# Kernel optimization log

Measured on AMD Instinct MI355X. Metric: run time of the kernel, lower is better.

## Reference

```python
import jax, jax.numpy as jnp
import numpy as np

B, T, E, V, L, BLK = 2, 2048, 1024, 32000, 12, 2048


def setup_inputs() -> dict:
    key = jax.random.key(0)
    ks = jax.random.split(key, 10)
    std = 0.005  # FHE-friendly tiny init, matches nn.init.normal_(std=0.005)
    init = lambda k, shape: jax.random.normal(k, shape, jnp.float32) * std
    return {
        "idx": jax.random.randint(ks[0], (B, T), 0, V, dtype=jnp.int32),
        "wte": init(ks[1], (V, E)),
        "wpe": init(ks[2], (BLK, E)),
        "ln1_w": jnp.ones((L, E), jnp.float32),   # FHELayerNorm weights init to ones
        "Wq": init(ks[3], (L, E, E)),
        "Wk": init(ks[4], (L, E, E)),
        "Wv": init(ks[5], (L, E, E)),
        "Wo": init(ks[6], (L, E, E)),
        "ln2_w": jnp.ones((L, E), jnp.float32),
        "fc1": init(ks[7], (L, 2 * E, E)),
        "fc2": init(ks[8], (L, E, 2 * E)),
        "lnf_w": jnp.ones((E,), jnp.float32),
        "lm_head": init(ks[9], (V, E)),
    }


def reference(idx, wte, wpe, ln1_w, Wq, Wk, Wv, Wo, ln2_w, fc1, fc2, lnf_w, lm_head):
    t = idx.shape[1]
    # embeddings, each scaled by 0.01
    x = wte[idx] * 0.01 + (wpe[:t] * 0.01)[None, :, :]  # [B,T,E]

    n_layer = ln1_w.shape[0]
    # inter-block rescale: 0.1 after every block except the last
    scales = jnp.where(jnp.arange(n_layer) < n_layer - 1, 0.1, 1.0).astype(x.dtype)

    def block(x, p):
        ln1, wq, wk, wv, wo, ln2, f1, f2, s = p
        # FHELayerNorm: pure scaling
        h = x * ln1 * 0.1
        # attention (single head over full E, softmax-free quadratic weights)
        q = jnp.einsum('bte,fe->btf', h, wq) * 0.01
        k = jnp.einsum('bte,fe->btf', h, wk) * 0.01
        v = jnp.einsum('bte,fe->btf', h, wv) * 0.1
        a = jnp.einsum('btf,bsf->bts', q, k) * 0.01      # [B,T,T]
        a = a * a * 0.1 + a * 0.1                         # pointwise quadratic
        ao = jnp.einsum('bts,bsf->btf', a, v) * 0.01
        attn_out = jnp.einsum('btf,ef->bte', ao, wo) * 0.1
        x = (x * 0.5 + attn_out * 0.5) * 0.1
        # MLP with polynomial activation
        h2 = x * ln2 * 0.1
        m = jnp.einsum('bte,fe->btf', h2, f1) * 0.05      # [B,T,2E]
        m = m * m * 0.1 + m * 0.1
        m = jnp.einsum('btf,ef->bte', m, f2) * 0.05
        x = (x * 0.5 + m * 0.5) * 0.1
        return x * s, None

    x, _ = jax.lax.scan(block, x, (ln1_w, Wq, Wk, Wv, Wo, ln2_w, fc1, fc2, scales))
    x = x * lnf_w * 0.1  # final FHELayerNorm
    logits = jnp.einsum('bte,ve->btv', x, lm_head) * 0.5
    return logits
```

## Files before the change

### kernel.cpp

```cpp
#include <hip/hip_runtime.h>
#include <hip/hip_fp8.h>
#include <stdint.h>
#include <math.h>

typedef unsigned short u16;
typedef __attribute__((ext_vector_type(8))) short bf16x8;
typedef __attribute__((ext_vector_type(4))) float f32x4;
typedef __attribute__((ext_vector_type(2))) long long llx2;

typedef __attribute__((address_space(1))) const uint32_t gas_u32;
typedef __attribute__((address_space(3))) uint32_t las_u32;

__device__ __forceinline__ u16 f2b(float f) {
  union { float f; uint32_t u; } v; v.f = f;
  uint32_t r = v.u + 0x7FFFu + ((v.u >> 16) & 1u);
  return (u16)(r >> 16);
}
__device__ __forceinline__ float b2f(u16 b) {
  union { uint32_t u; float f; } v; v.u = ((uint32_t)b) << 16; return v.f;
}
__device__ __forceinline__ uint8_t f8(float x) {
  __hip_fp8_e4m3 t(x);
  return (uint8_t)t.__x;
}
__device__ __forceinline__ int ipos(int k) {
  return (k & ~63) | (k & 7) | ((k & 32) >> 2) | ((k & 24) << 1);
}

__device__ __forceinline__ void gl_lds16(const void* g, void* l) {
  __builtin_amdgcn_global_load_lds((gas_u32*)g, (las_u32*)l, 16, 0, 0);
}
__device__ __forceinline__ void barrier_raw() {
  asm volatile("" ::: "memory");
  __builtin_amdgcn_s_barrier();
  asm volatile("" ::: "memory");
}

#define MM(A_, B_, C_)  __builtin_amdgcn_mfma_f32_16x16x32_bf16(A_, B_, C_, 0, 0, 0)
#define MM8(A_, B_, C_) __builtin_amdgcn_mfma_f32_16x16x32_fp8_fp8(A_, B_, C_, 0, 0, 0)

struct GP {
  const u16* A; long long asb;
  const u16* B[3]; long long bsb;
  u16* O[3]; long long osb;
  int M, N, K, lda, ldb, ldo;
  float alpha[3];
  int epi[3];
  int nsel, msel;
  float* fout; int ldf;
};

template <int MI>
__device__ __forceinline__ void epi_store(const GP& p, u16* __restrict__ Op, float alpha, int epi,
                                          int rbase0, int colb, const f32x4 (&acc)[MI][4], int l4, int l15) {
#pragma unroll
  for (int mi = 0; mi < MI; ++mi) {
    const int rbase = rbase0 + mi * 16 + l4 * 4;
#pragma unroll
    for (int ni = 0; ni < 4; ++ni) {
      const int col = colb + ni * 16 + l15;
      f32x4 v = acc[mi][ni];
#pragma unroll
      for (int r = 0; r < 4; ++r)
        Op[(size_t)(rbase + r) * p.ldo + col] = f2b(v[r] * alpha);
    }
  }
}

__device__ __forceinline__ void xcd_swz(int nwg, int orig, int gx, int& bx, int& by) {
  const int xcd = orig & 7, rem = orig >> 3;
  const int qq = nwg >> 3, rr = nwg & 7;
  const int wg = (xcd < rr ? xcd * (qq + 1) : rr * (qq + 1) + (xcd - rr) * qq) + rem;
  bx = wg % gx; by = wg / gx;
}

#define RD_A(off) do { \
  a0 = *(const bf16x8*)(Abase + (off));        a1 = *(const bf16x8*)(Abase + (off) + 1024); \
  a2 = *(const bf16x8*)(Abase + (off) + 2048); a3 = *(const bf16x8*)(Abase + (off) + 3072); \
} while (0)
#define RD_B(off) do { \
  b0 = *(const bf16x8*)(Bbase + (off));        b1 = *(const bf16x8*)(Bbase + (off) + 1024); \
  b2 = *(const bf16x8*)(Bbase + (off) + 2048); b3 = *(const bf16x8*)(Bbase + (off) + 3072); \
} while (0)
#define MF16(R) do { \
  acc[R+0][0]=MM(a0,b0,acc[R+0][0]); acc[R+0][1]=MM(a0,b1,acc[R+0][1]); acc[R+0][2]=MM(a0,b2,acc[R+0][2]); acc[R+0][3]=MM(a0,b3,acc[R+0][3]); \
  acc[R+1][0]=MM(a1,b0,acc[R+1][0]); acc[R+1][1]=MM(a1,b1,acc[R+1][1]); acc[R+1][2]=MM(a1,b2,acc[R+1][2]); acc[R+1][3]=MM(a1,b3,acc[R+1][3]); \
  acc[R+2][0]=MM(a2,b0,acc[R+2][0]); acc[R+2][1]=MM(a2,b1,acc[R+2][1]); acc[R+2][2]=MM(a2,b2,acc[R+2][2]); acc[R+2][3]=MM(a2,b3,acc[R+2][3]); \
  acc[R+3][0]=MM(a3,b0,acc[R+3][0]); acc[R+3][1]=MM(a3,b1,acc[R+3][1]); acc[R+3][2]=MM(a3,b2,acc[R+3][2]); acc[R+3][3]=MM(a3,b3,acc[R+3][3]); \
} while (0)

#define PHASE_MID() do { \
  asm volatile("s_waitcnt lgkmcnt(0)" ::: "memory"); \
  __builtin_amdgcn_sched_barrier(0); \
  __builtin_amdgcn_s_setprio(1); \
} while (0)
#define PHASE_END() do { \
  __builtin_amdgcn_s_setprio(0); \
  __builtin_amdgcn_sched_barrier(0); \
  barrier_raw(); \
} while (0)

#define SSA(q, kh, t) do { \
  gl_lds16(gA0 + (size_t)(t) * 64 + (kh) * 32, lAw + (q) * 32768 + (kh) * 8192); \
  gl_lds16(gA1 + (size_t)(t) * 64 + (kh) * 32, lAw + (q) * 32768 + (kh) * 8192 + 4096); \
} while (0)
#define SSB(q, kh, t) do { \
  gl_lds16(gB0 + (size_t)(t) * 64 + (kh) * 32, lBw + (q) * 32768 + (kh) * 8192); \
  gl_lds16(gB1 + (size_t)(t) * 64 + (kh) * 32, lBw + (q) * 32768 + (kh) * 8192 + 4096); \
} while (0)

__global__ __launch_bounds__(256, 2) void gemmS_k(GP p) {
  extern __shared__ __attribute__((aligned(16))) char lds[];
  const int z = blockIdx.z;
  int bx, by;
  xcd_swz(gridDim.x * gridDim.y, blockIdx.y * gridDim.x + blockIdx.x, gridDim.x, bx, by);
  const int m0 = bx * 128, n0 = by * 128;
  const u16* __restrict__ Ap = p.A + (size_t)z * p.asb;
  const u16* __restrict__ Bp = p.B[0] + (size_t)z * p.bsb;

  const int tid = threadIdx.x, wid = tid >> 6, lane = tid & 63;
  const int wm = wid >> 1, wn = wid & 1;
  const int l15 = lane & 15, l4 = lane >> 4;
  const int cswz16 = (l4 ^ ((l15 >> 1) & 3)) * 16;

  const f32x4 vzero = {0.f, 0.f, 0.f, 0.f};
  f32x4 acc[4][4];
#pragma unroll
  for (int i = 0; i < 4; ++i)
#pragma unroll
    for (int j = 0; j < 4; ++j) acc[i][j] = vzero;

  const int sr = lane >> 2;
  const int cg8 = ((lane & 3) ^ ((lane >> 3) & 3)) * 8;
  const u16* gA0 = Ap + (size_t)(m0 + wid * 16 + sr) * p.lda + cg8;
  const u16* gA1 = gA0 + (size_t)64 * p.lda;
  const u16* gB0 = Bp + (size_t)(n0 + wid * 16 + sr) * p.ldb + cg8;
  const u16* gB1 = gB0 + (size_t)64 * p.ldb;
  char* lAw = lds + wid * 1024;
  char* lBw = lds + 16384 + wid * 1024;

  const int nt = p.K >> 6;

  SSA(0, 0, 0); SSB(0, 0, 0); SSA(0, 1, 0); SSB(0, 1, 0);
  SSA(1, 0, 1); SSB(1, 0, 1);
  asm volatile("s_waitcnt vmcnt(4)" ::: "memory");
  barrier_raw();

  bf16x8 a0, a1, a2, a3, b0, b1, b2, b3;
  for (int t = 0; t < nt; ++t) {
    const int q = t & 1;
    const char* Abase = lds + q * 32768 + (wm * 64 + l15) * 64 + cswz16;
    const char* Bbase = lds + q * 32768 + 16384 + (wn * 64 + l15) * 64 + cswz16;
    RD_A(0); RD_B(0);
    if (t + 1 < nt) { SSA(q ^ 1, 1, t + 1); SSB(q ^ 1, 1, t + 1); }
    PHASE_MID(); MF16(0); PHASE_END();
    RD_A(8192); RD_B(8192);
    if (t + 2 < nt) { SSA(q, 0, t + 2); SSB(q, 0, t + 2); }
    PHASE_MID(); MF16(0);
    __builtin_amdgcn_s_setprio(0);
    __builtin_amdgcn_sched_barrier(0);
    if (t + 2 < nt) asm volatile("s_waitcnt vmcnt(4)" ::: "memory");
    else            asm volatile("s_waitcnt vmcnt(0)" ::: "memory");
    barrier_raw();
  }

  u16* Op = p.O[0] + (size_t)z * p.osb;
  epi_store<4>(p, Op, p.alpha[0], p.epi[0], m0 + wm * 64, n0 + wn * 64, acc, l4, l15);
}

struct GP8 {
  const uint8_t* A; long long asb;
  const uint8_t* B[3]; long long bsb;
  uint8_t* O[3]; long long osb;
  int K, lda, ldb, ldo;
  float m1[3], m2[3];
  int epi[3];
  int nsel, msel, nfirst;
  float qc;
  float* xres; const float* lnw; float rscale; float oscale;
  uint8_t* h8out;
  float* fout; int ldf;
};

#define S8A(q, kh, t) do { \
  gl_lds16(gA0 + (size_t)(t) * 128 + (kh) * 64, lAw + (q) * 32768 + (kh) * 8192); \
  gl_lds16(gA1 + (size_t)(t) * 128 + (kh) * 64, lAw + (q) * 32768 + (kh) * 8192 + 4096); \
} while (0)
#define S8B(q, kh, t) do { \
  gl_lds16(gB0 + (size_t)(t) * 128 + (kh) * 64, lBw + (q) * 32768 + (kh) * 8192); \
  gl_lds16(gB1 + (size_t)(t) * 128 + (kh) * 64, lBw + (q) * 32768 + (kh) * 8192 + 4096); \
} while (0)

#define MF8() do { \
  acc[0][0]=MM8(a0[0],b0[0],acc[0][0]); acc[0][0]=MM8(a0[1],b0[1],acc[0][0]); \
  acc[0][1]=MM8(a0[0],b1[0],acc[0][1]); acc[0][1]=MM8(a0[1],b1[1],acc[0][1]); \
  acc[0][2]=MM8(a0[0],b2[0],acc[0][2]); acc[0][2]=MM8(a0[1],b2[1],acc[0][2]); \
  acc[0][3]=MM8(a0[0],b3[0],acc[0][3]); acc[0][3]=MM8(a0[1],b3[1],acc[0][3]); \
  acc[1][0]=MM8(a1[0],b0[0],acc[1][0]); acc[1][0]=MM8(a1[1],b0[1],acc[1][0]); \
  acc[1][1]=MM8(a1[0],b1[0],acc[1][1]); acc[1][1]=MM8(a1[1],b1[1],acc[1][1]); \
  acc[1][2]=MM8(a1[0],b2[0],acc[1][2]); acc[1][2]=MM8(a1[1],b2[1],acc[1][2]); \
  acc[1][3]=MM8(a1[0],b3[0],acc[1][3]); acc[1][3]=MM8(a1[1],b3[1],acc[1][3]); \
  acc[2][0]=MM8(a2[0],b0[0],acc[2][0]); acc[2][0]=MM8(a2[1],b0[1],acc[2][0]); \
  acc[2][1]=MM8(a2[0],b1[0],acc[2][1]); acc[2][1]=MM8(a2[1],b1[1],acc[2][1]); \
  acc[2][2]=MM8(a2[0],b2[0],acc[2][2]); acc[2][2]=MM8(a2[1],b2[1],acc[2][2]); \
  acc[2][3]=MM8(a2[0],b3[0],acc[2][3]); acc[2][3]=MM8(a2[1],b3[1],acc[2][3]); \
  acc[3][0]=MM8(a3[0],b0[0],acc[3][0]); acc[3][0]=MM8(a3[1],b0[1],acc[3][0]); \
  acc[3][1]=MM8(a3[0],b1[0],acc[3][1]); acc[3][1]=MM8(a3[1],b1[1],acc[3][1]); \
  acc[3][2]=MM8(a3[0],b2[0],acc[3][2]); acc[3][2]=MM8(a3[1],b2[1],acc[3][2]); \
  acc[3][3]=MM8(a3[0],b3[0],acc[3][3]); acc[3][3]=MM8(a3[1],b3[1],acc[3][3]); \
} while (0)

__global__ __launch_bounds__(256, 2) void gemm8_k(GP8 p) {
  extern __shared__ __attribute__((aligned(16))) char lds[];
  const int z = blockIdx.z;
  int bx, by;
  xcd_swz(gridDim.x * gridDim.y, blockIdx.y * gridDim.x + blockIdx.x, gridDim.x, bx, by);
  const int m0 = p.nfirst ? by * 128 : bx * 128;
  const int n0 = p.nfirst ? bx * 128 : by * 128;
  const int zi = p.nsel ? (n0 >> 10) : 0;
  const int nB = p.nsel ? (n0 & 1023) : n0;
  const uint8_t* __restrict__ Ap = p.A + (size_t)z * p.asb;
  const uint8_t* __restrict__ Bp = p.B[zi] + (size_t)(p.msel ? (m0 >> 11) : z) * p.bsb;

  const int tid = threadIdx.x, wid = tid >> 6, lane = tid & 63;
  const int wm = wid >> 1, wn = wid & 1;
  const int l15 = lane & 15, l4 = lane >> 4;
  const int cswz16 = (l4 ^ ((l15 >> 1) & 3)) * 16;

  const f32x4 vzero = {0.f, 0.f, 0.f, 0.f};
  f32x4 acc[4][4];
#pragma unroll
  for (int i = 0; i < 4; ++i)
#pragma unroll
    for (int j = 0; j < 4; ++j) acc[i][j] = vzero;

  const int sr = lane >> 2;
  const int cgB = ((lane & 3) ^ ((lane >> 3) & 3)) * 16;
  const uint8_t* gA0 = Ap + (size_t)(m0 + wid * 16 + sr) * p.lda + cgB;
  const uint8_t* gA1 = gA0 + (size_t)64 * p.lda;
  const uint8_t* gB0 = Bp + (size_t)(nB + wid * 16 + sr) * p.ldb + cgB;
  const uint8_t* gB1 = gB0 + (size_t)64 * p.ldb;
  char* lAw = lds + wid * 1024;
  char* lBw = lds + 16384 + wid * 1024;

  const int nt = p.K >> 7;

  S8A(0, 0, 0); S8B(0, 0, 0); S8A(0, 1, 0); S8B(0, 1, 0);
  S8A(1, 0, 1); S8B(1, 0, 1);
  asm volatile("s_waitcnt vmcnt(4)" ::: "memory");
  barrier_raw();

  llx2 a0, a1, a2, a3, b0, b1, b2, b3;
  for (int t = 0; t < nt; ++t) {
    const int q = t & 1;
    const char* Abase = lds + q * 32768 + (wm * 64 + l15) * 64 + cswz16;
    const char* Bbase = lds + q * 32768 + 16384 + (wn * 64 + l15) * 64 + cswz16;
    a0 = *(const llx2*)Abase;          a1 = *(const llx2*)(Abase + 1024);
    a2 = *(const llx2*)(Abase + 2048); a3 = *(const llx2*)(Abase + 3072);
    b0 = *(const llx2*)Bbase;          b1 = *(const llx2*)(Bbase + 1024);
    b2 = *(const llx2*)(Bbase + 2048); b3 = *(const llx2*)(Bbase + 3072);
    if (t + 1 < nt) { S8A(q ^ 1, 1, t + 1); S8B(q ^ 1, 1, t + 1); }
    PHASE_MID(); MF8(); PHASE_END();
    a0 = *(const llx2*)(Abase + 8192);        a1 = *(const llx2*)(Abase + 8192 + 1024);
    a2 = *(const llx2*)(Abase + 8192 + 2048); a3 = *(const llx2*)(Abase + 8192 + 3072);
    b0 = *(const llx2*)(Bbase + 8192);        b1 = *(const llx2*)(Bbase + 8192 + 1024);
    b2 = *(const llx2*)(Bbase + 8192 + 2048); b3 = *(const llx2*)(Bbase + 8192 + 3072);
    if (t + 2 < nt) { S8A(q, 0, t + 2); S8B(q, 0, t + 2); }
    PHASE_MID(); MF8();
    __builtin_amdgcn_s_setprio(0);
    __builtin_amdgcn_sched_barrier(0);
    if (t + 2 < nt) asm volatile("s_waitcnt vmcnt(4)" ::: "memory");
    else            asm volatile("s_waitcnt vmcnt(0)" ::: "memory");
    barrier_raw();
  }

  const int epi = p.epi[zi];
  const float m1v = p.m1[zi], m2v = p.m2[zi];
  uint8_t* __restrict__ Op = p.O[zi] + (size_t)z * p.osb;
#pragma unroll
  for (int mi = 0; mi < 4; ++mi) {
    const int rbase = m0 + wm * 64 + mi * 16 + l4 * 4;
#pragma unroll
    for (int ni = 0; ni < 4; ++ni) {
      const int col = nB + wn * 64 + ni * 16 + l15;
      f32x4 v = acc[mi][ni];
      if (epi == 0) {
#pragma unroll
        for (int r = 0; r < 4; ++r) {
          float y = (v[r] * m1v) * m2v;
          Op[(size_t)(rbase + r) * p.ldo + ipos(col)] = f8(y);
        }
      } else if (epi == 1) {
        const int b = rbase >> 11, rb = rbase & 2047;
        uint32_t pk = 0;
#pragma unroll
        for (int r = 0; r < 4; ++r) {
          float y = (v[r] * m1v) * m2v;
          pk |= (uint32_t)f8(y) << (8 * r);
        }
        *(uint32_t*)(Op + (size_t)b * 2097152 + (size_t)col * 2048 + ipos(rb)) = pk;
      } else if (epi == 2) {
#pragma unroll
        for (int r = 0; r < 4; ++r) {
          float u = (v[r] * m1v) * m2v;
          Op[(size_t)(rbase + r) * p.ldo + ipos(col)] = f8(u * u * p.qc + u);
        }
      } else if (epi == 3) {
#pragma unroll
        for (int r = 0; r < 4; ++r) {
          float add = (v[r] * m1v) * m2v;
          size_t ix = (size_t)(rbase + r) * 1024 + col;
          float xn = (p.xres[ix] + add) * p.rscale;
          p.xres[ix] = xn;
          float hv = xn * p.lnw[col] * 0.1f;
          p.h8out[(size_t)(rbase + r) * 1024 + ipos(col)] = f8(hv * p.oscale);
        }
      } else {
#pragma unroll
        for (int r = 0; r < 4; ++r)
          __builtin_nontemporal_store((v[r] * m1v) * m2v,
                                      &p.fout[(size_t)(rbase + r) * p.ldf + col]);
      }
    }
  }
}

#define H8STAGE(b, t) do { \
  gl_lds16(gA0 + (size_t)(t) * 128,      lds + (b) * 24576 + wid * 1024); \
  gl_lds16(gB0 + (size_t)(t) * 128,      lds + (b) * 24576 + 8192 + wid * 1024); \
  gl_lds16(gB1 + (size_t)(t) * 128,      lds + (b) * 24576 + 12288 + wid * 1024); \
  gl_lds16(gA0 + (size_t)(t) * 128 + 64, lds + (b) * 24576 + 4096 + wid * 1024); \
  gl_lds16(gB0 + (size_t)(t) * 128 + 64, lds + (b) * 24576 + 16384 + wid * 1024); \
  gl_lds16(gB1 + (size_t)(t) * 128 + 64, lds + (b) * 24576 + 20480 + wid * 1024); \
} while (0)

#define MF8H(AK, BK_) do { \
  acc[0][0]=MM8(a0##AK[0],b0##BK_[0],acc[0][0]); acc[0][0]=MM8(a0##AK[1],b0##BK_[1],acc[0][0]); \
  acc[0][1]=MM8(a0##AK[0],b1##BK_[0],acc[0][1]); acc[0][1]=MM8(a0##AK[1],b1##BK_[1],acc[0][1]); \
  acc[0][2]=MM8(a0##AK[0],b2##BK_[0],acc[0][2]); acc[0][2]=MM8(a0##AK[1],b2##BK_[1],acc[0][2]); \
  acc[0][3]=MM8(a0##AK[0],b3##BK_[0],acc[0][3]); acc[0][3]=MM8(a0##AK[1],b3##BK_[1],acc[0][3]); \
  acc[1][0]=MM8(a1##AK[0],b0##BK_[0],acc[1][0]); acc[1][0]=MM8(a1##AK[1],b0##BK_[1],acc[1][0]); \
  acc[1][1]=MM8(a1##AK[0],b1##BK_[0],acc[1][1]); acc[1][1]=MM8(a1##AK[1],b1##BK_[1],acc[1][1]); \
  acc[1][2]=MM8(a1##AK[0],b2##BK_[0],acc[1][2]); acc[1][2]=MM8(a1##AK[1],b2##BK_[1],acc[1][2]); \
  acc[1][3]=MM8(a1##AK[0],b3##BK_[0],acc[1][3]); acc[1][3]=MM8(a1##AK[1],b3##BK_[1],acc[1][3]); \
} while (0)

__global__ __launch_bounds__(256, 2) void gemm8h_k(GP8 p) {
  extern __shared__ __attribute__((aligned(16))) char lds[];
  const int z = blockIdx.z;
  int bx, by;
  xcd_swz(gridDim.x * gridDim.y, blockIdx.y * gridDim.x + blockIdx.x, gridDim.x, bx, by);
  const int m0 = bx * 64, n0 = by * 128;
  const int zi = p.nsel ? (n0 >> 10) : 0;
  const int nB = p.nsel ? (n0 & 1023) : n0;
  const uint8_t* __restrict__ Ap = p.A + (size_t)z * p.asb;
  const uint8_t* __restrict__ Bp = p.B[zi] + (size_t)(p.msel ? (m0 >> 11) : z) * p.bsb;

  const int tid = threadIdx.x, wid = tid >> 6, lane = tid & 63;
  const int wm = wid >> 1, wn = wid & 1;
  const int l15 = lane & 15, l4 = lane >> 4;
  const int cswz16 = (l4 ^ ((l15 >> 1) & 3)) * 16;

  const f32x4 vzero = {0.f, 0.f, 0.f, 0.f};
  f32x4 acc[2][4];
#pragma unroll
  for (int i = 0; i < 2; ++i)
#pragma unroll
    for (int j = 0; j < 4; ++j) acc[i][j] = vzero;

  const int sr = lane >> 2;
  const int cgB = ((lane & 3) ^ ((lane >> 3) & 3)) * 16;
  const uint8_t* gA0 = Ap + (size_t)(m0 + wid * 16 + sr) * p.lda + cgB;
  const uint8_t* gB0 = Bp + (size_t)(nB + wid * 16 + sr) * p.ldb + cgB;
  const uint8_t* gB1 = gB0 + (size_t)64 * p.ldb;

  const int nt = p.K >> 7;

  H8STAGE(0, 0);
  H8STAGE(1, 1);
  asm volatile("s_waitcnt vmcnt(6)" ::: "memory");
  barrier_raw();

  int q = 0;
  for (int t = 0; t < nt; ++t) {
    const int bn = (q == 0) ? 2 : q - 1;
    const char* Abase = lds + q * 24576 + (wm * 32 + l15) * 64 + cswz16;
    const char* Bbase = lds + q * 24576 + 8192 + (wn * 64 + l15) * 64 + cswz16;
    llx2 a0k0 = *(const llx2*)Abase;
    llx2 a1k0 = *(const llx2*)(Abase + 1024);
    llx2 a0k1 = *(const llx2*)(Abase + 4096);
    llx2 a1k1 = *(const llx2*)(Abase + 4096 + 1024);
    llx2 b0k0 = *(const llx2*)Bbase;
    llx2 b1k0 = *(const llx2*)(Bbase + 1024);
    llx2 b2k0 = *(const llx2*)(Bbase + 2048);
    llx2 b3k0 = *(const llx2*)(Bbase + 3072);
    llx2 b0k1 = *(const llx2*)(Bbase + 8192);
    llx2 b1k1 = *(const llx2*)(Bbase + 8192 + 1024);
    llx2 b2k1 = *(const llx2*)(Bbase + 8192 + 2048);
    llx2 b3k1 = *(const llx2*)(Bbase + 8192 + 3072);
    if (t + 2 < nt) H8STAGE(bn, t + 2);
    asm volatile("s_waitcnt lgkmcnt(0)" ::: "memory");
    __builtin_amdgcn_sched_barrier(0);
    __builtin_amdgcn_s_setprio(1);
    MF8H(k0, k0);
    MF8H(k1, k1);
    __builtin_amdgcn_s_setprio(0);
    __builtin_amdgcn_sched_barrier(0);
    if (t + 2 < nt) asm volatile("s_waitcnt vmcnt(6)" ::: "memory");
    else            asm volatile("s_waitcnt vmcnt(0)" ::: "memory");
    barrier_raw();
    q = (q == 2) ? 0 : q + 1;
  }

  const int epi = p.epi[zi];
  const float m1v = p.m1[zi], m2v = p.m2[zi];
  uint8_t* __restrict__ Op = p.O[zi] + (size_t)z * p.osb;
#pragma unroll
  for (int mi = 0; mi < 2; ++mi) {
    const int rbase = m0 + wm * 32 + mi * 16 + l4 * 4;
#pragma unroll
    for (int ni = 0; ni < 4; ++ni) {
      const int col = nB + wn * 64 + ni * 16 + l15;
      f32x4 v = acc[mi][ni];
      if (epi == 0) {
#pragma unroll
        for (int r = 0; r < 4; ++r) {
          float y = (v[r] * m1v) * m2v;
          Op[(size_t)(rbase + r) * p.ldo + ipos(col)] = f8(y);
        }
      } else if (epi == 1) {
        const int b = rbase >> 11, rb = rbase & 2047;
        uint32_t pk = 0;
#pragma unroll
        for (int r = 0; r < 4; ++r) {
          float y = (v[r] * m1v) * m2v;
          pk |= (uint32_t)f8(y) << (8 * r);
        }
        *(uint32_t*)(Op + (size_t)b * 2097152 + (size_t)col * 2048 + ipos(rb)) = pk;
      } else if (epi == 2) {
#pragma unroll
        for (int r = 0; r < 4; ++r) {
          float u = (v[r] * m1v) * m2v;
          Op[(size_t)(rbase + r) * p.ldo + ipos(col)] = f8(u * u * p.qc + u);
        }
      } else if (epi == 3) {
#pragma unroll
        for (int r = 0; r < 4; ++r) {
          float add = (v[r] * m1v) * m2v;
          size_t ix = (size_t)(rbase + r) * 1024 + col;
          float xn = (p.xres[ix] + add) * p.rscale;
          p.xres[ix] = xn;
          float hv = xn * p.lnw[col] * 0.1f;
          p.h8out[(size_t)(rbase + r) * 1024 + ipos(col)] = f8(hv * p.oscale);
        }
      } else {
#pragma unroll
        for (int r = 0; r < 4; ++r)
          __builtin_nontemporal_store((v[r] * m1v) * m2v,
                                      &p.fout[(size_t)(rbase + r) * p.ldf + col]);
      }
    }
  }
}

__global__ __launch_bounds__(256) void embed8_k(const int* __restrict__ idx, const float* __restrict__ wte,
                                                const float* __restrict__ wpe, const float* __restrict__ ln1,
                                                float* __restrict__ x, uint8_t* __restrict__ h8, float sh) {
  const int bt = blockIdx.x;
  const int t = bt & 2047;
  const int tok = idx[bt];
  const int e = threadIdx.x * 4;
  const float4 wv = *(const float4*)(wte + (size_t)tok * 1024 + e);
  const float4 pv = *(const float4*)(wpe + (size_t)t * 1024 + e);
  const float4 lv = *(const float4*)(ln1 + e);
  float4 xo;
  xo.x = (wv.x + pv.x) * 0.01f;
  xo.y = (wv.y + pv.y) * 0.01f;
  xo.z = (wv.z + pv.z) * 0.01f;
  xo.w = (wv.w + pv.w) * 0.01f;
  *(float4*)(x + (size_t)bt * 1024 + e) = xo;
  uint32_t pk = (uint32_t)f8(xo.x * lv.x * 0.1f * sh)
              | ((uint32_t)f8(xo.y * lv.y * 0.1f * sh) << 8)
              | ((uint32_t)f8(xo.z * lv.z * 0.1f * sh) << 16)
              | ((uint32_t)f8(xo.w * lv.w * 0.1f * sh) << 24);
  *(uint32_t*)(h8 + (size_t)bt * 1024 + ipos(e)) = pk;
}

__global__ __launch_bounds__(256) void cvt_k(const float* __restrict__ src, u16* __restrict__ dst, long long n) {
  long long i = ((long long)blockIdx.x * 256 + threadIdx.x) * 8;
  const long long stride = (long long)gridDim.x * 256 * 8;
  for (; i < n; i += stride) {
    const float4 a = *(const float4*)(src + i);
    const float4 b = *(const float4*)(src + i + 4);
    bf16x8 o;
    o[0] = (short)f2b(a.x); o[1] = (short)f2b(a.y); o[2] = (short)f2b(a.z); o[3] = (short)f2b(a.w);
    o[4] = (short)f2b(b.x); o[5] = (short)f2b(b.y); o[6] = (short)f2b(b.z); o[7] = (short)f2b(b.w);
    *(bf16x8*)(dst + i) = o;
  }
}

__global__ __launch_bounds__(256) void cvtT_k(const float* __restrict__ src, u16* __restrict__ dst) {
  __shared__ float tl[64][68];
  const int z = blockIdx.z;
  const int c0 = blockIdx.x * 64, r0 = blockIdx.y * 64;
  const int tid = threadIdx.x;
  const float* s = src + (size_t)z * 1048576;
#pragma unroll
  for (int it = 0; it < 4; ++it) {
    const int r = it * 16 + (tid >> 4);
    const int c4 = (tid & 15) * 4;
    const float4 v = *(const float4*)(s + (size_t)(r0 + r) * 1024 + c0 + c4);
    tl[r][c4] = v.x; tl[r][c4 + 1] = v.y; tl[r][c4 + 2] = v.z; tl[r][c4 + 3] = v.w;
  }
  __syncthreads();
  const int c = tid >> 2;
  const int rr = (tid & 3) * 16;
  u16* d = dst + (size_t)z * 1048576 + (size_t)(c0 + c) * 1024 + r0 + rr;
  bf16x8 o0, o1;
#pragma unroll
  for (int j = 0; j < 8; ++j) o0[j] = (short)f2b(tl[rr + j][c]);
#pragma unroll
  for (int j = 0; j < 8; ++j) o1[j] = (short)f2b(tl[rr + 8 + j][c]);
  *(bf16x8*)d = o0;
  *(bf16x8*)(d + 8) = o1;
}

__global__ __launch_bounds__(256) void cvt8i_k(const u16* __restrict__ src, uint8_t* __restrict__ dst,
                                               long long n, float scale) {
  long long i = ((long long)blockIdx.x * 256 + threadIdx.x) * 8;
  const long long stride = (long long)gridDim.x * 256 * 8;
  for (; i < n; i += stride) {
    const bf16x8 v = *(const bf16x8*)(src + i);
    uint32_t lo = 0, hi = 0;
#pragma unroll
    for (int j = 0; j < 4; ++j) lo |= (uint32_t)f8(b2f((u16)v[j]) * scale) << (8 * j);
#pragma unroll
    for (int j = 0; j < 4; ++j) hi |= (uint32_t)f8(b2f((u16)v[4 + j]) * scale) << (8 * j);
    uint8_t* d = dst + ((i & ~63ll) | (((i >> 3) & 3) << 4) | (((i >> 5) & 1) << 3));
    *(uint32_t*)d = lo;
    *(uint32_t*)(d + 4) = hi;
  }
}

__global__ __launch_bounds__(256) void cvtf8i_k(const float* __restrict__ src, uint8_t* __restrict__ dst,
                                                long long n, float scale) {
  long long i = ((long long)blockIdx.x * 256 + threadIdx.x) * 8;
  const long long stride = (long long)gridDim.x * 256 * 8;
  for (; i < n; i += stride) {
    const float4 a = *(const float4*)(src + i);
    const float4 b = *(const float4*)(src + i + 4);
    uint32_t lo = (uint32_t)f8(a.x * scale) | ((uint32_t)f8(a.y * scale) << 8)
                | ((uint32_t)f8(a.z * scale) << 16) | ((uint32_t)f8(a.w * scale) << 24);
    uint32_t hi = (uint32_t)f8(b.x * scale) | ((uint32_t)f8(b.y * scale) << 8)
                | ((uint32_t)f8(b.z * scale) << 16) | ((uint32_t)f8(b.w * scale) << 24);
    uint8_t* d = dst + ((i & ~63ll) | (((i >> 3) & 3) << 4) | (((i >> 5) & 1) << 3));
    *(uint32_t*)d = lo;
    *(uint32_t*)(d + 4) = hi;
  }
}

__global__ __launch_bounds__(256) void megacvt8_k(const float* __restrict__ wq, const float* __restrict__ wk,
                                                  const float* __restrict__ f1, const float* __restrict__ f2,
                                                  uint8_t* __restrict__ dst, float scale) {
  const long long M1 = 1ll << 20;
  const long long per = 6 * M1;
  const long long total = 12 * per;
  long long i = ((long long)blockIdx.x * 256 + threadIdx.x) * 8;
  const long long stride = (long long)gridDim.x * 256 * 8;
  for (; i < total; i += stride) {
    const long long l = i / per;
    const long long off = i - l * per;
    const float* s; long long so;
    if      (off < M1)     { s = wq; so = l * M1 + off; }
    else if (off < 2 * M1) { s = wk; so = l * M1 + off - M1; }
    else if (off < 4 * M1) { s = f1; so = l * 2 * M1 + off - 2 * M1; }
    else                   { s = f2; so = l * 2 * M1 + off - 4 * M1; }
    const float4 a = *(const float4*)(s + so);
    const float4 b = *(const float4*)(s + so + 4);
    uint32_t lo = (uint32_t)f8(a.x * scale) | ((uint32_t)f8(a.y * scale) << 8)
                | ((uint32_t)f8(a.z * scale) << 16) | ((uint32_t)f8(a.w * scale) << 24);
    uint32_t hi = (uint32_t)f8(b.x * scale) | ((uint32_t)f8(b.y * scale) << 8)
                | ((uint32_t)f8(b.z * scale) << 16) | ((uint32_t)f8(b.w * scale) << 24);
    uint8_t* d = dst + ((i & ~63ll) | (((i >> 3) & 3) << 4) | (((i >> 5) & 1) << 3));
    *(uint32_t*)d = lo;
    *(uint32_t*)(d + 4) = hi;
  }
}

static inline double scp(double sigma) {
  double e = round(log2(0.5 / sigma));
  if (e > 120.0) e = 120.0;
  if (e < -120.0) e = -120.0;
  return ldexp(1.0, (int)e);
}
static inline void split2(double v, float& a, float& b) {
  if (v == 0.0) { a = 0.f; b = 0.f; return; }
  int e; frexp(v, &e);
  int h = e / 2;
  a = (float)ldexp(1.0, h);
  b = (float)ldexp(v, -h);
}

extern "C" void kernel_launch(void* const* d_in, const int* in_sizes, int n_in,
                              void* d_out, int out_size, void* d_ws, size_t ws_size,
                              hipStream_t stream) {
  const int*   idx  = (const int*)  d_in[0];
  const float* wte  = (const float*)d_in[1];
  const float* wpe  = (const float*)d_in[2];
  const float* ln1w = (const float*)d_in[3];
  const float* Wq   = (const float*)d_in[4];
  const float* Wk   = (const float*)d_in[5];
  const float* Wv   = (const float*)d_in[6];
  const float* Wo   = (const float*)d_in[7];
  const float* ln2w = (const float*)d_in[8];
  const float* fc1  = (const float*)d_in[9];
  const float* fc2  = (const float*)d_in[10];
  const float* lnfw = (const float*)d_in[11];
  const float* lmh  = (const float*)d_in[12];
  float* out = (float*)d_out;

  double dSh1[12], dSqk[12], dSaq[12], dSu[12], dSh2[12], dSmq[12], dShF;
  {
    double sx = 7e-5;
    for (int l = 0; l < 12; ++l) {
      double sh1 = sx * 0.1;
      double sq  = sh1 * 0.005 * 32.0 * 0.01;
      double saq = 32.0 * sq * sq * 0.01 * 0.1;
      double su  = sh1 * 8e-4 * 32.0 * 0.1;
      double sx2 = sx * 0.05;
      double sh2 = sx2 * 0.1;
      double smq = sh2 * 0.005 * 32.0 * 0.05 * 0.1;
      dSh1[l] = scp(sh1); dSqk[l] = scp(sq); dSaq[l] = scp(saq);
      dSu[l] = scp(su); dSh2[l] = scp(sh2); dSmq[l] = scp(smq);
      sx = sx2 * 0.05 * (l < 11 ? 0.1 : 1.0);
    }
    dShF = scp(sx * 0.1);
  }
  const double SW = 128.0, SWVO = 512.0, SF = 128.0, SL = 128.0;

  char* w = (char*)d_ws;
  float*   x    = (float*)w;    w += (size_t)4096 * 1024 * 4;
  uint8_t* h8   = (uint8_t*)w;  w += (size_t)4096 * 1024;
  uint8_t* q8   = (uint8_t*)w;  w += (size_t)4096 * 1024;
  uint8_t* k8   = (uint8_t*)w;  w += (size_t)4096 * 1024;
  uint8_t* uT8  = (uint8_t*)w;  w += (size_t)2 * 1024 * 2048;
  uint8_t* a8   = (uint8_t*)w;  w += (size_t)2 * 2048 * 2048;
  uint8_t* mb8  = (uint8_t*)w;  w += (size_t)4096 * 2048;
  uint8_t* lw8  = (uint8_t*)w;  w += (size_t)12 * 6291456;
  uint8_t* wvo8 = (uint8_t*)w;  w += (size_t)12 * 1048576;
  uint8_t* lmh8 = q8;
  u16* WvT   = (u16*)lw8;
  u16* WoB   = (u16*)(lw8 + 25165824);
  u16* Wvo16 = (u16*)(lw8 + 50331648);

  const size_t SHS = 65536, SH8 = 65536, SHH = 73728;

  embed8_k<<<4096, 256, 0, stream>>>(idx, wte, wpe, ln1w, x, h8, (float)dSh1[0]);

  cvtT_k<<<dim3(16, 16, 12), 256, 0, stream>>>(Wv, WvT);
  cvt_k<<<2048, 256, 0, stream>>>(Wo, WoB, 12ll * 1048576);
  {
    GP p{};
    p.A = WoB; p.asb = 1048576;
    p.B[0] = WvT; p.bsb = 1048576;
    p.O[0] = Wvo16; p.osb = 1048576;
    p.M = 1024; p.N = 1024; p.K = 1024; p.lda = 1024; p.ldb = 1024; p.ldo = 1024;
    p.alpha[0] = 1.0f; p.epi[0] = 0;
    gemmS_k<<<dim3(8, 8, 12), 256, SHS, stream>>>(p);
  }
  cvt8i_k<<<2048, 256, 0, stream>>>(Wvo16, wvo8, 12ll * 1048576, (float)SWVO);
  megacvt8_k<<<2048, 256, 0, stream>>>(Wq, Wk, fc1, fc2, lw8, (float)SW);

  for (int l = 0; l < 12; ++l) {
    uint8_t* lwl = lw8 + (size_t)l * 6291456;
    {
      GP8 p{};
      p.A = h8; p.asb = 0;
      p.B[0] = lwl; p.B[1] = lwl + 1048576; p.B[2] = wvo8 + (size_t)l * 1048576; p.bsb = 0;
      p.O[0] = q8; p.O[1] = k8; p.O[2] = uT8; p.osb = 0;
      p.K = 1024; p.lda = 1024; p.ldb = 1024; p.ldo = 1024;
      split2(0.01 * dSqk[l] / (dSh1[l] * SW), p.m1[0], p.m2[0]);
      p.m1[1] = p.m1[0]; p.m2[1] = p.m2[0];
      split2(0.1 * dSu[l] / (dSh1[l] * SWVO), p.m1[2], p.m2[2]);
      p.epi[0] = 0; p.epi[1] = 0; p.epi[2] = 1;
      p.nsel = 1;
      gemm8h_k<<<dim3(64, 24, 1), 256, SHH, stream>>>(p);
    }
    {
      GP8 p{};
      p.A = q8; p.asb = 2097152;
      p.B[0] = k8; p.bsb = 2097152;
      p.O[0] = a8; p.osb = 4194304;
      p.K = 1024; p.lda = 1024; p.ldb = 1024; p.ldo = 2048;
      split2(0.001 * dSaq[l] / (dSqk[l] * dSqk[l]), p.m1[0], p.m2[0]);
      p.qc = (float)(10.0 / dSaq[l]);
      p.epi[0] = 2;
      gemm8_k<<<dim3(16, 16, 2), 256, SH8, stream>>>(p);
    }
    {
      GP8 p{};
      p.A = a8; p.asb = 0;
      p.B[0] = uT8; p.bsb = 2097152; p.msel = 1;
      p.O[0] = a8; p.osb = 0;
      p.K = 2048; p.lda = 2048; p.ldb = 2048; p.ldo = 1024;
      split2(0.001 / (dSaq[l] * dSu[l]), p.m1[0], p.m2[0]);
      p.epi[0] = 3;
      p.xres = x; p.lnw = ln2w + (size_t)l * 1024; p.rscale = 0.05f;
      p.oscale = (float)dSh2[l]; p.h8out = h8;
      gemm8h_k<<<dim3(64, 8, 1), 256, SHH, stream>>>(p);
    }
    {
      GP8 p{};
      p.A = h8; p.asb = 0;
      p.B[0] = lwl + 2097152; p.bsb = 0;
      p.O[0] = mb8; p.osb = 0;
      p.K = 1024; p.lda = 1024; p.ldb = 1024; p.ldo = 2048;
      split2(0.005 * dSmq[l] / (dSh2[l] * SF), p.m1[0], p.m2[0]);
      p.qc = (float)(10.0 / dSmq[l]);
      p.epi[0] = 2;
      gemm8_k<<<dim3(32, 16, 1), 256, SH8, stream>>>(p);
    }
    {
      GP8 p{};
      p.A = mb8; p.asb = 0;
      p.B[0] = lwl + 4194304; p.bsb = 0;
      p.O[0] = mb8; p.osb = 0;
      p.K = 2048; p.lda = 2048; p.ldb = 2048; p.ldo = 1024;
      split2(0.05 / (dSmq[l] * SF), p.m1[0], p.m2[0]);
      p.epi[0] = 3;
      p.xres = x;
      p.rscale = (l < 11) ? 0.005f : 0.05f;
      if (l < 11) { p.lnw = ln1w + (size_t)(l + 1) * 1024; p.oscale = (float)dSh1[l + 1]; }
      else        { p.lnw = lnfw; p.oscale = (float)dShF; }
      p.h8out = h8;
      gemm8h_k<<<dim3(64, 8, 1), 256, SHH, stream>>>(p);
    }
  }

  cvtf8i_k<<<2048, 256, 0, stream>>>(lmh, lmh8, 32768000ll, (float)SL);
  {
    GP8 p{};
    p.A = h8; p.asb = 0;
    p.B[0] = lmh8; p.bsb = 0;
    p.O[0] = lmh8; p.osb = 0;
    p.K = 1024; p.lda = 1024; p.ldb = 1024; p.ldo = 0;
    split2(0.5 / (dShF * SL), p.m1[0], p.m2[0]);
    p.epi[0] = 4;
    p.nfirst = 1;
    p.fout = out; p.ldf = 32000;
    gemm8_k<<<dim3(250, 32, 1), 256, SH8, stream>>>(p);
  }
}
```

Measured before the change: 2.045 ms.

## Compute fused Wo·Wv weight product in FP8 and switch QKV projection kernel

The per-layer Wo·Wv weight product is now computed with the FP8 GEMM kernel on FP8-quantized, transposed inputs. Before, both weights were converted to bf16, multiplied with a separate bf16 GEMM, and the result was re-quantized to FP8. This removes the bf16 conversion kernels, the bf16 GEMM and the extra re-quantization pass. The per-layer fused QKV projection also moves from the gemm8h kernel to gemm8_k with a different grid shape. The risk is accuracy loss from quantizing both weight factors to FP8 before the product, and a possibly less tuned tile configuration for the QKV projection.

```diff
diff --git a/kernel.cpp b/kernel.cpp
--- a/kernel.cpp
+++ b/kernel.cpp
@@ -4,21 +4,12 @@
 #include <math.h>
 
 typedef unsigned short u16;
-typedef __attribute__((ext_vector_type(8))) short bf16x8;
 typedef __attribute__((ext_vector_type(4))) float f32x4;
 typedef __attribute__((ext_vector_type(2))) long long llx2;
 
 typedef __attribute__((address_space(1))) const uint32_t gas_u32;
 typedef __attribute__((address_space(3))) uint32_t las_u32;
 
-__device__ __forceinline__ u16 f2b(float f) {
-  union { float f; uint32_t u; } v; v.f = f;
-  uint32_t r = v.u + 0x7FFFu + ((v.u >> 16) & 1u);
-  return (u16)(r >> 16);
-}
-__device__ __forceinline__ float b2f(u16 b) {
-  union { uint32_t u; float f; } v; v.u = ((uint32_t)b) << 16; return v.f;
-}
 __device__ __forceinline__ uint8_t f8(float x) {
   __hip_fp8_e4m3 t(x);
   return (uint8_t)t.__x;
@@ -36,58 +27,7 @@
   asm volatile("" ::: "memory");
 }
 
-#define MM(A_, B_, C_)  __builtin_amdgcn_mfma_f32_16x16x32_bf16(A_, B_, C_, 0, 0, 0)
 #define MM8(A_, B_, C_) __builtin_amdgcn_mfma_f32_16x16x32_fp8_fp8(A_, B_, C_, 0, 0, 0)
-
-struct GP {
-  const u16* A; long long asb;
-  const u16* B[3]; long long bsb;
-  u16* O[3]; long long osb;
-  int M, N, K, lda, ldb, ldo;
-  float alpha[3];
-  int epi[3];
-  int nsel, msel;
-  float* fout; int ldf;
-};
-
-template <int MI>
-__device__ __forceinline__ void epi_store(const GP& p, u16* __restrict__ Op, float alpha, int epi,
-                                          int rbase0, int colb, const f32x4 (&acc)[MI][4], int l4, int l15) {
-#pragma unroll
-  for (int mi = 0; mi < MI; ++mi) {
-    const int rbase = rbase0 + mi * 16 + l4 * 4;
-#pragma unroll
-    for (int ni = 0; ni < 4; ++ni) {
-      const int col = colb + ni * 16 + l15;
-      f32x4 v = acc[mi][ni];
-#pragma unroll
-      for (int r = 0; r < 4; ++r)
-        Op[(size_t)(rbase + r) * p.ldo + col] = f2b(v[r] * alpha);
-    }
-  }
-}
-
-__device__ __forceinline__ void xcd_swz(int nwg, int orig, int gx, int& bx, int& by) {
-  const int xcd = orig & 7, rem = orig >> 3;
-  const int qq = nwg >> 3, rr = nwg & 7;
-  const int wg = (xcd < rr ? xcd * (qq + 1) : rr * (qq + 1) + (xcd - rr) * qq) + rem;
-  bx = wg % gx; by = wg / gx;
-}
-
-#define RD_A(off) do { \
-  a0 = *(const bf16x8*)(Abase + (off));        a1 = *(const bf16x8*)(Abase + (off) + 1024); \
-  a2 = *(const bf16x8*)(Abase + (off) + 2048); a3 = *(const bf16x8*)(Abase + (off) + 3072); \
-} while (0)
-#define RD_B(off) do { \
-  b0 = *(const bf16x8*)(Bbase + (off));        b1 = *(const bf16x8*)(Bbase + (off) + 1024); \
-  b2 = *(const bf16x8*)(Bbase + (off) + 2048); b3 = *(const bf16x8*)(Bbase + (off) + 3072); \
-} while (0)
-#define MF16(R) do { \
-  acc[R+0][0]=MM(a0,b0,acc[R+0][0]); acc[R+0][1]=MM(a0,b1,acc[R+0][1]); acc[R+0][2]=MM(a0,b2,acc[R+0][2]); acc[R+0][3]=MM(a0,b3,acc[R+0][3]); \
-  acc[R+1][0]=MM(a1,b0,acc[R+1][0]); acc[R+1][1]=MM(a1,b1,acc[R+1][1]); acc[R+1][2]=MM(a1,b2,acc[R+1][2]); acc[R+1][3]=MM(a1,b3,acc[R+1][3]); \
-  acc[R+2][0]=MM(a2,b0,acc[R+2][0]); acc[R+2][1]=MM(a2,b1,acc[R+2][1]); acc[R+2][2]=MM(a2,b2,acc[R+2][2]); acc[R+2][3]=MM(a2,b3,acc[R+2][3]); \
-  acc[R+3][0]=MM(a3,b0,acc[R+3][0]); acc[R+3][1]=MM(a3,b1,acc[R+3][1]); acc[R+3][2]=MM(a3,b2,acc[R+3][2]); acc[R+3][3]=MM(a3,b3,acc[R+3][3]); \
-} while (0)
 
 #define PHASE_MID() do { \
   asm volatile("s_waitcnt lgkmcnt(0)" ::: "memory"); \
@@ -100,72 +40,11 @@
   barrier_raw(); \
 } while (0)
 
-#define SSA(q, kh, t) do { \
-  gl_lds16(gA0 + (size_t)(t) * 64 + (kh) * 32, lAw + (q) * 32768 + (kh) * 8192); \
-  gl_lds16(gA1 + (size_t)(t) * 64 + (kh) * 32, lAw + (q) * 32768 + (kh) * 8192 + 4096); \
-} while (0)
-#define SSB(q, kh, t) do { \
-  gl_lds16(gB0 + (size_t)(t) * 64 + (kh) * 32, lBw + (q) * 32768 + (kh) * 8192); \
-  gl_lds16(gB1 + (size_t)(t) * 64 + (kh) * 32, lBw + (q) * 32768 + (kh) * 8192 + 4096); \
-} while (0)
-
-__global__ __launch_bounds__(256, 2) void gemmS_k(GP p) {
-  extern __shared__ __attribute__((aligned(16))) char lds[];
-  const int z = blockIdx.z;
-  int bx, by;
-  xcd_swz(gridDim.x * gridDim.y, blockIdx.y * gridDim.x + blockIdx.x, gridDim.x, bx, by);
-  const int m0 = bx * 128, n0 = by * 128;
-  const u16* __restrict__ Ap = p.A + (size_t)z * p.asb;
-  const u16* __restrict__ Bp = p.B[0] + (size_t)z * p.bsb;
-
-  const int tid = threadIdx.x, wid = tid >> 6, lane = tid & 63;
-  const int wm = wid >> 1, wn = wid & 1;
-  const int l15 = lane & 15, l4 = lane >> 4;
-  const int cswz16 = (l4 ^ ((l15 >> 1) & 3)) * 16;
-
-  const f32x4 vzero = {0.f, 0.f, 0.f, 0.f};
-  f32x4 acc[4][4];
-#pragma unroll
-  for (int i = 0; i < 4; ++i)
-#pragma unroll
-    for (int j = 0; j < 4; ++j) acc[i][j] = vzero;
-
-  const int sr = lane >> 2;
-  const int cg8 = ((lane & 3) ^ ((lane >> 3) & 3)) * 8;
-  const u16* gA0 = Ap + (size_t)(m0 + wid * 16 + sr) * p.lda + cg8;
-  const u16* gA1 = gA0 + (size_t)64 * p.lda;
-  const u16* gB0 = Bp + (size_t)(n0 + wid * 16 + sr) * p.ldb + cg8;
-  const u16* gB1 = gB0 + (size_t)64 * p.ldb;
-  char* lAw = lds + wid * 1024;
-  char* lBw = lds + 16384 + wid * 1024;
-
-  const int nt = p.K >> 6;
-
-  SSA(0, 0, 0); SSB(0, 0, 0); SSA(0, 1, 0); SSB(0, 1, 0);
-  SSA(1, 0, 1); SSB(1, 0, 1);
-  asm volatile("s_waitcnt vmcnt(4)" ::: "memory");
-  barrier_raw();
-
-  bf16x8 a0, a1, a2, a3, b0, b1, b2, b3;
-  for (int t = 0; t < nt; ++t) {
-    const int q = t & 1;
-    const char* Abase = lds + q * 32768 + (wm * 64 + l15) * 64 + cswz16;
-    const char* Bbase = lds + q * 32768 + 16384 + (wn * 64 + l15) * 64 + cswz16;
-    RD_A(0); RD_B(0);
-    if (t + 1 < nt) { SSA(q ^ 1, 1, t + 1); SSB(q ^ 1, 1, t + 1); }
-    PHASE_MID(); MF16(0); PHASE_END();
-    RD_A(8192); RD_B(8192);
-    if (t + 2 < nt) { SSA(q, 0, t + 2); SSB(q, 0, t + 2); }
-    PHASE_MID(); MF16(0);
-    __builtin_amdgcn_s_setprio(0);
-    __builtin_amdgcn_sched_barrier(0);
-    if (t + 2 < nt) asm volatile("s_waitcnt vmcnt(4)" ::: "memory");
-    else            asm volatile("s_waitcnt vmcnt(0)" ::: "memory");
-    barrier_raw();
-  }
-
-  u16* Op = p.O[0] + (size_t)z * p.osb;
-  epi_store<4>(p, Op, p.alpha[0], p.epi[0], m0 + wm * 64, n0 + wn * 64, acc, l4, l15);
+__device__ __forceinline__ void xcd_swz(int nwg, int orig, int gx, int& bx, int& by) {
+  const int xcd = orig & 7, rem = orig >> 3;
+  const int qq = nwg >> 3, rr = nwg & 7;
+  const int wg = (xcd < rr ? xcd * (qq + 1) : rr * (qq + 1) + (xcd - rr) * qq) + rem;
+  bx = wg % gx; by = wg / gx;
 }
 
 struct GP8 {
@@ -486,20 +365,8 @@
   *(uint32_t*)(h8 + (size_t)bt * 1024 + ipos(e)) = pk;
 }
 
-__global__ __launch_bounds__(256) void cvt_k(const float* __restrict__ src, u16* __restrict__ dst, long long n) {
-  long long i = ((long long)blockIdx.x * 256 + threadIdx.x) * 8;
-  const long long stride = (long long)gridDim.x * 256 * 8;
-  for (; i < n; i += stride) {
-    const float4 a = *(const float4*)(src + i);
-    const float4 b = *(const float4*)(src + i + 4);
-    bf16x8 o;
-    o[0] = (short)f2b(a.x); o[1] = (short)f2b(a.y); o[2] = (short)f2b(a.z); o[3] = (short)f2b(a.w);
-    o[4] = (short)f2b(b.x); o[5] = (short)f2b(b.y); o[6] = (short)f2b(b.z); o[7] = (short)f2b(b.w);
-    *(bf16x8*)(dst + i) = o;
-  }
-}
-
-__global__ __launch_bounds__(256) void cvtT_k(const float* __restrict__ src, u16* __restrict__ dst) {
+__global__ __launch_bounds__(256) void cvtT8_k(const float* __restrict__ src, uint8_t* __restrict__ dst,
+                                               float scale) {
   __shared__ float tl[64][68];
   const int z = blockIdx.z;
   const int c0 = blockIdx.x * 64, r0 = blockIdx.y * 64;
@@ -515,31 +382,20 @@
   __syncthreads();
   const int c = tid >> 2;
   const int rr = (tid & 3) * 16;
-  u16* d = dst + (size_t)z * 1048576 + (size_t)(c0 + c) * 1024 + r0 + rr;
-  bf16x8 o0, o1;
-#pragma unroll
-  for (int j = 0; j < 8; ++j) o0[j] = (short)f2b(tl[rr + j][c]);
-#pragma unroll
-  for (int j = 0; j < 8; ++j) o1[j] = (short)f2b(tl[rr + 8 + j][c]);
-  *(bf16x8*)d = o0;
-  *(bf16x8*)(d + 8) = o1;
-}
-
-__global__ __launch_bounds__(256) void cvt8i_k(const u16* __restrict__ src, uint8_t* __restrict__ dst,
-                                               long long n, float scale) {
-  long long i = ((long long)blockIdx.x * 256 + threadIdx.x) * 8;
-  const long long stride = (long long)gridDim.x * 256 * 8;
-  for (; i < n; i += stride) {
-    const bf16x8 v = *(const bf16x8*)(src + i);
-    uint32_t lo = 0, hi = 0;
-#pragma unroll
-    for (int j = 0; j < 4; ++j) lo |= (uint32_t)f8(b2f((u16)v[j]) * scale) << (8 * j);
-#pragma unroll
-    for (int j = 0; j < 4; ++j) hi |= (uint32_t)f8(b2f((u16)v[4 + j]) * scale) << (8 * j);
-    uint8_t* d = dst + ((i & ~63ll) | (((i >> 3) & 3) << 4) | (((i >> 5) & 1) << 3));
-    *(uint32_t*)d = lo;
-    *(uint32_t*)(d + 4) = hi;
-  }
+  const int base = r0 + rr;
+  const int O = (base & ~63) | ((base & 32) >> 2) | ((base & 16) << 1);
+  uint8_t* d = dst + (size_t)z * 1048576 + (size_t)(c0 + c) * 1024 + O;
+  uint32_t w0 = 0, w1 = 0, w2 = 0, w3 = 0;
+#pragma unroll
+  for (int j = 0; j < 4; ++j) w0 |= (uint32_t)f8(tl[rr + j][c] * scale) << (8 * j);
+#pragma unroll
+  for (int j = 0; j < 4; ++j) w1 |= (uint32_t)f8(tl[rr + 4 + j][c] * scale) << (8 * j);
+#pragma unroll
+  for (int j = 0; j < 4; ++j) w2 |= (uint32_t)f8(tl[rr + 8 + j][c] * scale) << (8 * j);
+#pragma unroll
+  for (int j = 0; j < 4; ++j) w3 |= (uint32_t)f8(tl[rr + 12 + j][c] * scale) << (8 * j);
+  *(uint32_t*)d = w0;        *(uint32_t*)(d + 4) = w1;
+  *(uint32_t*)(d + 16) = w2; *(uint32_t*)(d + 20) = w3;
 }
 
 __global__ __launch_bounds__(256) void cvtf8i_k(const float* __restrict__ src, uint8_t* __restrict__ dst,
@@ -649,26 +505,25 @@
   uint8_t* lw8  = (uint8_t*)w;  w += (size_t)12 * 6291456;
   uint8_t* wvo8 = (uint8_t*)w;  w += (size_t)12 * 1048576;
   uint8_t* lmh8 = q8;
-  u16* WvT   = (u16*)lw8;
-  u16* WoB   = (u16*)(lw8 + 25165824);
-  u16* Wvo16 = (u16*)(lw8 + 50331648);
-
-  const size_t SHS = 65536, SH8 = 65536, SHH = 73728;
+  uint8_t* wvT8 = lw8;
+  uint8_t* wo8  = lw8 + 25165824;
+
+  const size_t SH8 = 65536, SHH = 73728;
 
   embed8_k<<<4096, 256, 0, stream>>>(idx, wte, wpe, ln1w, x, h8, (float)dSh1[0]);
 
-  cvtT_k<<<dim3(16, 16, 12), 256, 0, stream>>>(Wv, WvT);
-  cvt_k<<<2048, 256, 0, stream>>>(Wo, WoB, 12ll * 1048576);
+  cvtT8_k<<<dim3(16, 16, 12), 256, 0, stream>>>(Wv, wvT8, (float)SW);
+  cvtf8i_k<<<2048, 256, 0, stream>>>(Wo, wo8, 12ll * 1048576, (float)SW);
   {
-    GP p{};
-    p.A = WoB; p.asb = 1048576;
-    p.B[0] = WvT; p.bsb = 1048576;
-    p.O[0] = Wvo16; p.osb = 1048576;
-    p.M = 1024; p.N = 1024; p.K = 1024; p.lda = 1024; p.ldb = 1024; p.ldo = 1024;
-    p.alpha[0] = 1.0f; p.epi[0] = 0;
-    gemmS_k<<<dim3(8, 8, 12), 256, SHS, stream>>>(p);
-  }
-  cvt8i_k<<<2048, 256, 0, stream>>>(Wvo16, wvo8, 12ll * 1048576, (float)SWVO);
+    GP8 p{};
+    p.A = wo8; p.asb = 1048576;
+    p.B[0] = wvT8; p.bsb = 1048576;
+    p.O[0] = wvo8; p.osb = 1048576;
+    p.K = 1024; p.lda = 1024; p.ldb = 1024; p.ldo = 1024;
+    split2(SWVO / (SW * SW), p.m1[0], p.m2[0]);
+    p.epi[0] = 0;
+    gemm8_k<<<dim3(8, 8, 12), 256, SH8, stream>>>(p);
+  }
   megacvt8_k<<<2048, 256, 0, stream>>>(Wq, Wk, fc1, fc2, lw8, (float)SW);
 
   for (int l = 0; l < 12; ++l) {
@@ -684,7 +539,7 @@
       split2(0.1 * dSu[l] / (dSh1[l] * SWVO), p.m1[2], p.m2[2]);
       p.epi[0] = 0; p.epi[1] = 0; p.epi[2] = 1;
       p.nsel = 1;
-      gemm8h_k<<<dim3(64, 24, 1), 256, SHH, stream>>>(p);
+      gemm8_k<<<dim3(32, 24, 1), 256, SH8, stream>>>(p);
     }
     {
       GP8 p{};
```

Measured after the change: 1.971 ms. 1.04x faster.
